# Kernel optimization log

Hardware: AMD Instinct MI355X
Metric: run time of the kernel (lower is better)

## Reference

```python
import jax, jax.numpy as jnp
import numpy as np

D_IN = 512
D_HID = 512
D_OUT = 512
N = 32768


def hamilton_Wq(Wr, Wi, Wj, Wk, xr, xi, xj, xk):
    """Quaternion Hamilton product h = W (x) q, W: [out,in], x*: [N,in] -> [N,out].
    Implemented as one block-structured GEMM: stack inputs along feature dim and
    contract against the sign-structured 4x4 block weight matrix.
    """
    # x_cat: [N, 4*in]
    x_cat = jnp.concatenate([xr, xi, xj, xk], axis=-1)
    # Block rows correspond to input components (r,i,j,k), block cols to output components.
    # h_r = xr@Wr^T - xi@Wi^T - xj@Wj^T - xk@Wk^T
    # h_i = xr@Wi^T + xi@Wr^T + xj@Wk^T - xk@Wj^T
    # h_j = xr@Wj^T - xi@Wk^T + xj@Wr^T + xk@Wi^T
    # h_k = xr@Wk^T + xi@Wj^T - xj@Wi^T + xk@Wr^T
    W_block = jnp.concatenate([
        jnp.concatenate([Wr, Wi, Wj, Wk], axis=0),      # multiplies xr
        jnp.concatenate([-Wi, Wr, -Wk, Wj], axis=0),    # multiplies xi
        jnp.concatenate([-Wj, Wk, Wr, -Wi], axis=0),    # multiplies xj
        jnp.concatenate([-Wk, -Wj, Wi, Wr], axis=0),    # multiplies xk
    ], axis=1)  # [4*out, 4*in]
    h = jnp.einsum('ni,oi->no', x_cat, W_block)  # [N, 4*out]
    out = Wr.shape[0]
    return h[:, :out], h[:, out:2 * out], h[:, 2 * out:3 * out], h[:, 3 * out:]


def setup_inputs() -> dict:
    key = jax.random.key(0)
    ks = jax.random.split(key, 12)
    inp = {
        'q_r': jax.random.normal(ks[0], (N, D_IN), jnp.float32),
        'q_i': jax.random.normal(ks[1], (N, D_IN), jnp.float32),
        'q_j': jax.random.normal(ks[2], (N, D_IN), jnp.float32),
        'q_k': jax.random.normal(ks[3], (N, D_IN), jnp.float32),
    }
    s1 = 1.0 / np.sqrt(D_IN)
    s2 = 1.0 / np.sqrt(D_HID)
    for n, (ki, sh, sc) in {
        'W1_r': (ks[4], (D_HID, D_IN), s1), 'W1_i': (ks[5], (D_HID, D_IN), s1),
        'W1_j': (ks[6], (D_HID, D_IN), s1), 'W1_k': (ks[7], (D_HID, D_IN), s1),
        'W2_r': (ks[8], (D_OUT, D_HID), s2), 'W2_i': (ks[9], (D_OUT, D_HID), s2),
        'W2_j': (ks[10], (D_OUT, D_HID), s2), 'W2_k': (ks[11], (D_OUT, D_HID), s2),
    }.items():
        inp[n] = jax.random.normal(ki, sh, jnp.float32) * sc
    inp['b1_r'] = jnp.zeros((D_HID,), jnp.float32)
    inp['b1_i'] = jnp.full((D_HID,), 0.2, jnp.float32)
    inp['b1_j'] = jnp.full((D_HID,), 0.2, jnp.float32)
    inp['b1_k'] = jnp.full((D_HID,), 0.2, jnp.float32)
    inp['b2_r'] = jnp.zeros((D_OUT,), jnp.float32)
    inp['b2_i'] = jnp.full((D_OUT,), 0.2, jnp.float32)
    inp['b2_j'] = jnp.full((D_OUT,), 0.2, jnp.float32)
    inp['b2_k'] = jnp.full((D_OUT,), 0.2, jnp.float32)
    return inp


def reference(q_r, q_i, q_j, q_k,
              W1_r, W1_i, W1_j, W1_k, b1_r, b1_i, b1_j, b1_k,
              W2_r, W2_i, W2_j, W2_k, b2_r, b2_i, b2_j, b2_k):
    # layer 1: Hamilton product + bias + componentwise ReLU
    hr, hi, hj, hk = hamilton_Wq(W1_r, W1_i, W1_j, W1_k, q_r, q_i, q_j, q_k)
    hr = jax.nn.relu(hr + b1_r)
    hi = jax.nn.relu(hi + b1_i)
    hj = jax.nn.relu(hj + b1_j)
    hk = jax.nn.relu(hk + b1_k)
    # layer 2: Hamilton product + bias
    or_, oi, oj, ok = hamilton_Wq(W2_r, W2_i, W2_j, W2_k, hr, hi, hj, hk)
    return (or_ + b2_r, oi + b2_i, oj + b2_j, ok + b2_k)
```

## Files before the change

kernel.cpp:

```cpp
#include <hip/hip_runtime.h>
#include <hip/hip_bf16.h>

#define N_ROWS 32768
#define DQ 512
#define DC 2048
#define KDIM 2048

typedef float f32x4 __attribute__((ext_vector_type(4)));
typedef short bf16x8 __attribute__((ext_vector_type(8)));

__global__ void pack_w_kernel(const float* __restrict__ Wr, const float* __restrict__ Wi,
                              const float* __restrict__ Wj, const float* __restrict__ Wk,
                              __hip_bfloat16* __restrict__ Wblk) {
    int idx = blockIdx.x * blockDim.x + threadIdx.x;
    int base = idx * 4;
    int o = base >> 11;
    int i = base & 2047;
    int ob = o >> 9, ib = i >> 9;
    int oo = o & 511, ii = i & 511;
    int s = ob ^ ib;
    const float* src = (s == 0) ? Wr : (s == 1) ? Wi : (s == 2) ? Wj : Wk;
    float sgn = ((0x428E >> (ob * 4 + ib)) & 1) ? -1.0f : 1.0f;
    float4 v = *(const float4*)(src + oo * 512 + ii);
    __hip_bfloat16 outv[4];
    outv[0] = __float2bfloat16(sgn * v.x);
    outv[1] = __float2bfloat16(sgn * v.y);
    outv[2] = __float2bfloat16(sgn * v.z);
    outv[3] = __float2bfloat16(sgn * v.w);
    *(uint2*)(Wblk + base) = *(uint2*)outv;
}

__global__ void pack_bias_kernel(const float* __restrict__ b1r, const float* __restrict__ b1i,
                                 const float* __restrict__ b1j, const float* __restrict__ b1k,
                                 const float* __restrict__ b2r, const float* __restrict__ b2i,
                                 const float* __restrict__ b2j, const float* __restrict__ b2k,
                                 float* __restrict__ b1full, float* __restrict__ b2full) {
    int idx = blockIdx.x * blockDim.x + threadIdx.x;
    int c = idx >> 9, d = idx & 511;
    const float* s1 = (c == 0) ? b1r : (c == 1) ? b1i : (c == 2) ? b1j : b1k;
    const float* s2 = (c == 0) ? b2r : (c == 1) ? b2i : (c == 2) ? b2j : b2k;
    b1full[idx] = s1[d];
    b2full[idx] = s2[d];
}

__global__ void pack_x_kernel(const float* __restrict__ qr, const float* __restrict__ qi,
                              const float* __restrict__ qj, const float* __restrict__ qk,
                              __hip_bfloat16* __restrict__ xcat) {
    int idx = blockIdx.x * blockDim.x + threadIdx.x;
    size_t base = (size_t)idx * 8;
    int col = (int)(base & 2047);
    size_t n = base >> 11;
    int c = col >> 9, d = col & 511;
    const float* src = (c == 0) ? qr : (c == 1) ? qi : (c == 2) ? qj : qk;
    const float* p = src + n * 512 + d;
    float4 v0 = *(const float4*)(p);
    float4 v1 = *(const float4*)(p + 4);
    __hip_bfloat16 o[8];
    o[0] = __float2bfloat16(v0.x); o[1] = __float2bfloat16(v0.y);
    o[2] = __float2bfloat16(v0.z); o[3] = __float2bfloat16(v0.w);
    o[4] = __float2bfloat16(v1.x); o[5] = __float2bfloat16(v1.y);
    o[6] = __float2bfloat16(v1.z); o[7] = __float2bfloat16(v1.w);
    *(uint4*)(xcat + base) = *(uint4*)o;
}

template <int MODE>
__global__ __launch_bounds__(512, 2) void qgemm8_kernel(
    const __hip_bfloat16* __restrict__ A,
    const __hip_bfloat16* __restrict__ B,
    const float* __restrict__ bias,
    void* __restrict__ Cout, int M)
{
    constexpr int NT = KDIM / 64;
    __shared__ short lds[2][4][8192];

    const int t = threadIdx.x;
    const int lane = t & 63;
    const int wv = t >> 6;
    const int wrow = wv >> 2;
    const int wcol = wv & 3;
    const int lm = lane & 15;

    const int m0 = blockIdx.y * 256;
    const int n0 = blockIdx.x * 256;

    const short* Ag = (const short*)A;
    const short* Bg = (const short*)B;

    const int swzb = (lane & 7) << 4;
    const int cbs0 = ((((lane >> 4) << 4)) ^ swzb) >> 1;
    const int cbs1 = ((64 + ((lane >> 4) << 4)) ^ swzb) >> 1;

    const int srow = (wv << 3) + (lane >> 3);
    const int secol = ((lane & 7) ^ (lane >> 3)) << 3;

    auto STAGE = [&](const short* G, int grow, int kk, short* region) {
        const short* g0 = G + (size_t)(grow + srow) * KDIM + kk + secol;
        __builtin_amdgcn_global_load_lds(
            (const __attribute__((address_space(1))) void*)g0,
            (__attribute__((address_space(3))) void*)(region + wv * 512), 16, 0, 0);
        __builtin_amdgcn_global_load_lds(
            (const __attribute__((address_space(1))) void*)(g0 + (size_t)64 * KDIM),
            (__attribute__((address_space(3))) void*)(region + 4096 + wv * 512), 16, 0, 0);
    };

    f32x4 acc[8][4] = {};
    bf16x8 af[2][4], bl[2][2], bh[2][2];

    STAGE(Ag, m0, 0, lds[0][0]);
    STAGE(Ag, m0 + 128, 0, lds[0][1]);
    STAGE(Bg, n0, 0, lds[0][2]);
    STAGE(Bg, n0 + 128, 0, lds[0][3]);
    STAGE(Bg, n0, 64, lds[1][2]);
    STAGE(Bg, n0 + 128, 64, lds[1][3]);
    asm volatile("s_waitcnt vmcnt(4)" ::: "memory");
    __builtin_amdgcn_s_barrier();

    for (int u = 0; u < NT; ++u) {
        const int b = u & 1;
        const short* aR = lds[b][wrow];
        const short* bR = lds[b][2 + (wcol >> 1)];
        const int kk = u * 64;
        const int rBb = (wcol & 1) * 64;

#pragma unroll
        for (int mi = 0; mi < 4; mi++) {
            const short* p = aR + (mi * 16 + lm) * 64;
            af[0][mi] = *(const bf16x8*)(p + cbs0);
            af[1][mi] = *(const bf16x8*)(p + cbs1);
        }
#pragma unroll
        for (int ni = 0; ni < 2; ni++) {
            const short* p = bR + (rBb + ni * 16 + lm) * 64;
            bl[0][ni] = *(const bf16x8*)(p + cbs0);
            bl[1][ni] = *(const bf16x8*)(p + cbs1);
        }
#pragma unroll
        for (int ni = 0; ni < 2; ni++) {
            const short* p = bR + (rBb + 32 + ni * 16 + lm) * 64;
            bh[0][ni] = *(const bf16x8*)(p + cbs0);
            bh[1][ni] = *(const bf16x8*)(p + cbs1);
        }
        if (u < NT - 1) {
            STAGE(Ag, m0, kk + 64, lds[b ^ 1][0]);
            STAGE(Ag, m0 + 128, kk + 64, lds[b ^ 1][1]);
        }
        __builtin_amdgcn_s_setprio(1);
#pragma unroll
        for (int ks = 0; ks < 2; ks++)
#pragma unroll
            for (int mi = 0; mi < 4; mi++)
#pragma unroll
                for (int ni = 0; ni < 2; ni++)
                    acc[mi][ni] = __builtin_amdgcn_mfma_f32_16x16x32_bf16(
                        af[ks][mi], bl[ks][ni], acc[mi][ni], 0, 0, 0);
#pragma unroll
        for (int ks = 0; ks < 2; ks++)
#pragma unroll
            for (int mi = 0; mi < 4; mi++)
#pragma unroll
                for (int ni = 0; ni < 2; ni++)
                    acc[mi][2 + ni] = __builtin_amdgcn_mfma_f32_16x16x32_bf16(
                        af[ks][mi], bh[ks][ni], acc[mi][2 + ni], 0, 0, 0);
        __builtin_amdgcn_s_setprio(0);
        __builtin_amdgcn_s_barrier();

#pragma unroll
        for (int mi = 0; mi < 4; mi++) {
            const short* p = aR + (64 + mi * 16 + lm) * 64;
            af[0][mi] = *(const bf16x8*)(p + cbs0);
            af[1][mi] = *(const bf16x8*)(p + cbs1);
        }
        if (u < NT - 2) {
            STAGE(Bg, n0, kk + 128, lds[b][2]);
            STAGE(Bg, n0 + 128, kk + 128, lds[b][3]);
        }
        __builtin_amdgcn_s_setprio(1);
#pragma unroll
        for (int ks = 0; ks < 2; ks++)
#pragma unroll
            for (int mi = 0; mi < 4; mi++)
#pragma unroll
                for (int ni = 0; ni < 2; ni++)
                    acc[4 + mi][ni] = __builtin_amdgcn_mfma_f32_16x16x32_bf16(
                        af[ks][mi], bl[ks][ni], acc[4 + mi][ni], 0, 0, 0);
#pragma unroll
        for (int ks = 0; ks < 2; ks++)
#pragma unroll
            for (int mi = 0; mi < 4; mi++)
#pragma unroll
                for (int ni = 0; ni < 2; ni++)
                    acc[4 + mi][2 + ni] = __builtin_amdgcn_mfma_f32_16x16x32_bf16(
                        af[ks][mi], bh[ks][ni], acc[4 + mi][2 + ni], 0, 0, 0);
        __builtin_amdgcn_s_setprio(0);
        if (u < NT - 2)      { asm volatile("s_waitcnt vmcnt(4)" ::: "memory"); }
        else if (u == NT - 2){ asm volatile("s_waitcnt vmcnt(0)" ::: "memory"); }
        __builtin_amdgcn_s_barrier();
    }

#pragma unroll
    for (int mi8 = 0; mi8 < 8; mi8++) {
#pragma unroll
        for (int ni4 = 0; ni4 < 4; ni4++) {
            const int n_g = n0 + wcol * 64 + ni4 * 16 + lm;
            const float bia = bias[n_g];
#pragma unroll
            for (int r = 0; r < 4; r++) {
                const int m_g = m0 + wrow * 128 + (mi8 >> 2) * 64 + (mi8 & 3) * 16 + (lane >> 4) * 4 + r;
                float v = acc[mi8][ni4][r] + bia;
                if (MODE == 0) {
                    v = fmaxf(v, 0.0f);
                    ((__hip_bfloat16*)Cout)[(size_t)m_g * DC + n_g] = __float2bfloat16(v);
                } else {
                    const int c = n_g >> 9, d = n_g & 511;
                    ((float*)Cout)[(size_t)c * ((size_t)M * DQ) + (size_t)m_g * DQ + d] = v;
                }
            }
        }
    }
}

extern "C" void kernel_launch(void* const* d_in, const int* in_sizes, int n_in,
                              void* d_out, int out_size, void* d_ws, size_t ws_size,
                              hipStream_t stream) {
    const float* qr = (const float*)d_in[0];
    const float* qi = (const float*)d_in[1];
    const float* qj = (const float*)d_in[2];
    const float* qk = (const float*)d_in[3];
    const float* W1r = (const float*)d_in[4];
    const float* W1i = (const float*)d_in[5];
    const float* W1j = (const float*)d_in[6];
    const float* W1k = (const float*)d_in[7];
    const float* W2r = (const float*)d_in[8];
    const float* W2i = (const float*)d_in[9];
    const float* W2j = (const float*)d_in[10];
    const float* W2k = (const float*)d_in[11];
    const float* b1r = (const float*)d_in[12];
    const float* b1i = (const float*)d_in[13];
    const float* b1j = (const float*)d_in[14];
    const float* b1k = (const float*)d_in[15];
    const float* b2r = (const float*)d_in[16];
    const float* b2i = (const float*)d_in[17];
    const float* b2j = (const float*)d_in[18];
    const float* b2k = (const float*)d_in[19];

    char* ws = (char*)d_ws;
    __hip_bfloat16* W1blk = (__hip_bfloat16*)ws;
    __hip_bfloat16* W2blk = (__hip_bfloat16*)(ws + (8u << 20));
    float* b1full = (float*)(ws + (16u << 20));
    float* b2full = b1full + 2048;
    __hip_bfloat16* xcat = (__hip_bfloat16*)(ws + (16u << 20) + 65536);
    __hip_bfloat16* H = xcat + (size_t)N_ROWS * DC;

    pack_w_kernel<<<(2048 * 2048 / 4) / 256, 256, 0, stream>>>(W1r, W1i, W1j, W1k, W1blk);
    pack_w_kernel<<<(2048 * 2048 / 4) / 256, 256, 0, stream>>>(W2r, W2i, W2j, W2k, W2blk);
    pack_bias_kernel<<<8, 256, 0, stream>>>(b1r, b1i, b1j, b1k, b2r, b2i, b2j, b2k, b1full, b2full);
    pack_x_kernel<<<(N_ROWS * (size_t)DC / 8) / 256, 256, 0, stream>>>(qr, qi, qj, qk, xcat);

    dim3 grid(DC / 256, N_ROWS / 256);
    qgemm8_kernel<0><<<grid, 512, 0, stream>>>(xcat, W1blk, b1full, (void*)H, N_ROWS);
    qgemm8_kernel<1><<<grid, 512, 0, stream>>>(H, W2blk, b2full, d_out, N_ROWS);
}
```

Measured before the change: 935.6 us.

## Restructure GEMM main loop into k-split halves with single wait per tile

Replaces the ping-pong schedule, which split the tile into two M-halves with staggered A/B prefetch, with a simpler double buffer. Each iteration waits for all loads, then computes the full 256x256 tile in two k-halves of 32, issuing the next A prefetch after the first fragment reads and the next B prefetch after the second. This drops one barrier per iteration and simplifies the fragment layout, so each wave now owns 8 contiguous 16-row M fragments. The cost is a full vmcnt(0) wait at the top of each iteration, which exposes load latency that the earlier staggered B prefetch had hidden.

```diff
diff --git a/kernel.cpp b/kernel.cpp
--- a/kernel.cpp
+++ b/kernel.cpp
@@ -71,7 +71,7 @@
     void* __restrict__ Cout, int M)
 {
     constexpr int NT = KDIM / 64;
-    __shared__ short lds[2][4][8192];
+    __shared__ short lds[2][2][16384];
 
     const int t = threadIdx.x;
     const int lane = t & 63;
@@ -93,108 +93,64 @@
     const int srow = (wv << 3) + (lane >> 3);
     const int secol = ((lane & 7) ^ (lane >> 3)) << 3;
 
-    auto STAGE = [&](const short* G, int grow, int kk, short* region) {
-        const short* g0 = G + (size_t)(grow + srow) * KDIM + kk + secol;
-        __builtin_amdgcn_global_load_lds(
-            (const __attribute__((address_space(1))) void*)g0,
-            (__attribute__((address_space(3))) void*)(region + wv * 512), 16, 0, 0);
-        __builtin_amdgcn_global_load_lds(
-            (const __attribute__((address_space(1))) void*)(g0 + (size_t)64 * KDIM),
-            (__attribute__((address_space(3))) void*)(region + 4096 + wv * 512), 16, 0, 0);
+    auto STAGE4 = [&](const short* G, int grow, int kk, short* region) {
+#pragma unroll
+        for (int i = 0; i < 4; i++) {
+            __builtin_amdgcn_global_load_lds(
+                (const __attribute__((address_space(1))) void*)
+                    (G + (size_t)(grow + srow + i * 64) * KDIM + kk + secol),
+                (__attribute__((address_space(3))) void*)(region + i * 4096 + wv * 512),
+                16, 0, 0);
+        }
     };
 
     f32x4 acc[8][4] = {};
-    bf16x8 af[2][4], bl[2][2], bh[2][2];
-
-    STAGE(Ag, m0, 0, lds[0][0]);
-    STAGE(Ag, m0 + 128, 0, lds[0][1]);
-    STAGE(Bg, n0, 0, lds[0][2]);
-    STAGE(Bg, n0 + 128, 0, lds[0][3]);
-    STAGE(Bg, n0, 64, lds[1][2]);
-    STAGE(Bg, n0 + 128, 64, lds[1][3]);
-    asm volatile("s_waitcnt vmcnt(4)" ::: "memory");
-    __builtin_amdgcn_s_barrier();
+
+    STAGE4(Ag, m0, 0, lds[0][0]);
+    STAGE4(Bg, n0, 0, lds[0][1]);
 
     for (int u = 0; u < NT; ++u) {
         const int b = u & 1;
-        const short* aR = lds[b][wrow];
-        const short* bR = lds[b][2 + (wcol >> 1)];
+        const short* aR = lds[b][0];
+        const short* bR = lds[b][1];
         const int kk = u * 64;
-        const int rBb = (wcol & 1) * 64;
-
-#pragma unroll
-        for (int mi = 0; mi < 4; mi++) {
-            const short* p = aR + (mi * 16 + lm) * 64;
-            af[0][mi] = *(const bf16x8*)(p + cbs0);
-            af[1][mi] = *(const bf16x8*)(p + cbs1);
-        }
-#pragma unroll
-        for (int ni = 0; ni < 2; ni++) {
-            const short* p = bR + (rBb + ni * 16 + lm) * 64;
-            bl[0][ni] = *(const bf16x8*)(p + cbs0);
-            bl[1][ni] = *(const bf16x8*)(p + cbs1);
-        }
-#pragma unroll
-        for (int ni = 0; ni < 2; ni++) {
-            const short* p = bR + (rBb + 32 + ni * 16 + lm) * 64;
-            bh[0][ni] = *(const bf16x8*)(p + cbs0);
-            bh[1][ni] = *(const bf16x8*)(p + cbs1);
-        }
-        if (u < NT - 1) {
-            STAGE(Ag, m0, kk + 64, lds[b ^ 1][0]);
-            STAGE(Ag, m0 + 128, kk + 64, lds[b ^ 1][1]);
-        }
+
+        asm volatile("s_waitcnt vmcnt(0)" ::: "memory");
+        __builtin_amdgcn_s_barrier();
+
+        bf16x8 af[8], bfr[4];
+
+#pragma unroll
+        for (int mi = 0; mi < 8; mi++)
+            af[mi] = *(const bf16x8*)(aR + (wrow * 128 + mi * 16 + lm) * 64 + cbs0);
+#pragma unroll
+        for (int ni = 0; ni < 4; ni++)
+            bfr[ni] = *(const bf16x8*)(bR + (wcol * 64 + ni * 16 + lm) * 64 + cbs0);
+        if (u < NT - 1) STAGE4(Ag, m0, kk + 64, lds[b ^ 1][0]);
         __builtin_amdgcn_s_setprio(1);
 #pragma unroll
-        for (int ks = 0; ks < 2; ks++)
-#pragma unroll
-            for (int mi = 0; mi < 4; mi++)
-#pragma unroll
-                for (int ni = 0; ni < 2; ni++)
-                    acc[mi][ni] = __builtin_amdgcn_mfma_f32_16x16x32_bf16(
-                        af[ks][mi], bl[ks][ni], acc[mi][ni], 0, 0, 0);
-#pragma unroll
-        for (int ks = 0; ks < 2; ks++)
-#pragma unroll
-            for (int mi = 0; mi < 4; mi++)
-#pragma unroll
-                for (int ni = 0; ni < 2; ni++)
-                    acc[mi][2 + ni] = __builtin_amdgcn_mfma_f32_16x16x32_bf16(
-                        af[ks][mi], bh[ks][ni], acc[mi][2 + ni], 0, 0, 0);
+        for (int mi = 0; mi < 8; mi++)
+#pragma unroll
+            for (int ni = 0; ni < 4; ni++)
+                acc[mi][ni] = __builtin_amdgcn_mfma_f32_16x16x32_bf16(
+                    af[mi], bfr[ni], acc[mi][ni], 0, 0, 0);
         __builtin_amdgcn_s_setprio(0);
-        __builtin_amdgcn_s_barrier();
-
-#pragma unroll
-        for (int mi = 0; mi < 4; mi++) {
-            const short* p = aR + (64 + mi * 16 + lm) * 64;
-            af[0][mi] = *(const bf16x8*)(p + cbs0);
-            af[1][mi] = *(const bf16x8*)(p + cbs1);
-        }
-        if (u < NT - 2) {
-            STAGE(Bg, n0, kk + 128, lds[b][2]);
-            STAGE(Bg, n0 + 128, kk + 128, lds[b][3]);
-        }
+
+#pragma unroll
+        for (int mi = 0; mi < 8; mi++)
+            af[mi] = *(const bf16x8*)(aR + (wrow * 128 + mi * 16 + lm) * 64 + cbs1);
+#pragma unroll
+        for (int ni = 0; ni < 4; ni++)
+            bfr[ni] = *(const bf16x8*)(bR + (wcol * 64 + ni * 16 + lm) * 64 + cbs1);
+        if (u < NT - 1) STAGE4(Bg, n0, kk + 64, lds[b ^ 1][1]);
         __builtin_amdgcn_s_setprio(1);
 #pragma unroll
-        for (int ks = 0; ks < 2; ks++)
-#pragma unroll
-            for (int mi = 0; mi < 4; mi++)
-#pragma unroll
-                for (int ni = 0; ni < 2; ni++)
-                    acc[4 + mi][ni] = __builtin_amdgcn_mfma_f32_16x16x32_bf16(
-                        af[ks][mi], bl[ks][ni], acc[4 + mi][ni], 0, 0, 0);
-#pragma unroll
-        for (int ks = 0; ks < 2; ks++)
-#pragma unroll
-            for (int mi = 0; mi < 4; mi++)
-#pragma unroll
-                for (int ni = 0; ni < 2; ni++)
-                    acc[4 + mi][2 + ni] = __builtin_amdgcn_mfma_f32_16x16x32_bf16(
-                        af[ks][mi], bh[ks][ni], acc[4 + mi][2 + ni], 0, 0, 0);
+        for (int mi = 0; mi < 8; mi++)
+#pragma unroll
+            for (int ni = 0; ni < 4; ni++)
+                acc[mi][ni] = __builtin_amdgcn_mfma_f32_16x16x32_bf16(
+                    af[mi], bfr[ni], acc[mi][ni], 0, 0, 0);
         __builtin_amdgcn_s_setprio(0);
-        if (u < NT - 2)      { asm volatile("s_waitcnt vmcnt(4)" ::: "memory"); }
-        else if (u == NT - 2){ asm volatile("s_waitcnt vmcnt(0)" ::: "memory"); }
-        __builtin_amdgcn_s_barrier();
     }
 
 #pragma unroll
@@ -205,7 +161,7 @@
             const float bia = bias[n_g];
 #pragma unroll
             for (int r = 0; r < 4; r++) {
-                const int m_g = m0 + wrow * 128 + (mi8 >> 2) * 64 + (mi8 & 3) * 16 + (lane >> 4) * 4 + r;
+                const int m_g = m0 + wrow * 128 + mi8 * 16 + (lane >> 4) * 4 + r;
                 float v = acc[mi8][ni4][r] + bia;
                 if (MODE == 0) {
                     v = fmaxf(v, 0.0f);
```

Measured after the change: 973.9 us. 4.1% more time.
